# Optimization experiments

Hardware: AMD Instinct MI355X
Metric: run time of the kernel (lower is better)

Reference implementation:

```python
import jax, jax.numpy as jnp
import numpy as np

D_MODEL, N_HEADS, D_LLM = 1024, 16, 4096
D_KEYS = D_MODEL // N_HEADS  # 64


def setup_inputs() -> dict:
    key = jax.random.key(0)
    ks = jax.random.split(key, 11)
    s = lambda fan_in: 1.0 / np.sqrt(fan_in)
    inp = {
        "target_embedding": jax.random.normal(ks[0], (4, 2048, D_MODEL), jnp.float32),
        "source_embedding": jax.random.normal(ks[1], (4, 1024, D_LLM), jnp.float32),
        "value_embedding": jax.random.normal(ks[2], (4, 1024, D_LLM), jnp.float32),
        "Wq": jax.random.uniform(ks[3], (D_MODEL, D_KEYS * N_HEADS), jnp.float32, -s(D_MODEL), s(D_MODEL)),
        "bq": jax.random.uniform(ks[4], (D_KEYS * N_HEADS,), jnp.float32, -s(D_MODEL), s(D_MODEL)),
        "Wk": jax.random.uniform(ks[5], (D_LLM, D_KEYS * N_HEADS), jnp.float32, -s(D_LLM), s(D_LLM)),
        "bk": jax.random.uniform(ks[6], (D_KEYS * N_HEADS,), jnp.float32, -s(D_LLM), s(D_LLM)),
        "Wv": jax.random.uniform(ks[7], (D_LLM, D_KEYS * N_HEADS), jnp.float32, -s(D_LLM), s(D_LLM)),
        "bv": jax.random.uniform(ks[8], (D_KEYS * N_HEADS,), jnp.float32, -s(D_LLM), s(D_LLM)),
        "Wo": jax.random.uniform(ks[9], (D_KEYS * N_HEADS, D_MODEL), jnp.float32, -s(D_KEYS * N_HEADS), s(D_KEYS * N_HEADS)),
        "bo": jax.random.uniform(ks[10], (D_MODEL,), jnp.float32, -s(D_KEYS * N_HEADS), s(D_KEYS * N_HEADS)),
    }
    return inp


def reference(target_embedding, source_embedding, value_embedding,
              Wq, bq, Wk, bk, Wv, bv, Wo, bo):
    B, L, _ = target_embedding.shape
    _, S, _ = source_embedding.shape
    H, E = N_HEADS, D_KEYS
    q = (target_embedding @ Wq + bq).reshape(B, L, H, E)
    k = (source_embedding @ Wk + bk).reshape(B, S, H, E)
    v = (value_embedding @ Wv + bv).reshape(B, S, H, E)
    scale = 1.0 / np.sqrt(E)
    scores = jnp.einsum('blhe,bshe->bhls', q, k)  # [B,H,L,S]
    A = jax.nn.softmax(scale * scores, axis=-1)   # dropout = identity (eval mode)
    out = jnp.einsum('bhls,bshe->blhe', A, v).reshape(B, L, H * E)
    return out @ Wo + bo
```

## Files before the change

kernel.cpp:

```cpp
#include <hip/hip_runtime.h>
#include <hip/hip_bf16.h>

using bf16 = __hip_bfloat16;
typedef __attribute__((ext_vector_type(8))) short short8;
typedef __attribute__((ext_vector_type(4))) float f32x4;

static constexpr int Bc = 4, Lc = 2048, Sc = 1024;
static constexpr int DModel = 1024;

__device__ __forceinline__ void gload16(const void* g, void* l) {
  __builtin_amdgcn_global_load_lds((const __attribute__((address_space(1))) void*)g,
                                   (__attribute__((address_space(3))) void*)l,
                                   16, 0, 0);
}

__device__ __forceinline__ void wait_vm3()  { asm volatile("s_waitcnt vmcnt(3)" ::: "memory"); }
__device__ __forceinline__ void wait_vm0()  { asm volatile("s_waitcnt vmcnt(0)" ::: "memory"); }
__device__ __forceinline__ void barrier_raw() { asm volatile("s_barrier" ::: "memory"); }

__global__ __launch_bounds__(256) void prep(
    const float* __restrict__ Wq, bf16* __restrict__ WqT,
    const float* __restrict__ Wk, bf16* __restrict__ WkT,
    const float* __restrict__ Wv, bf16* __restrict__ WvT,
    const float* __restrict__ Wo, bf16* __restrict__ WoT,
    const float* __restrict__ a, bf16* __restrict__ ao, long na4,
    const float* __restrict__ b, bf16* __restrict__ bo, long nb4,
    const float* __restrict__ c, bf16* __restrict__ co, long nc4) {
  __shared__ bf16 tile[32][33];
  int bid = blockIdx.x;
  if (bid < 10240) {
    const float* in; bf16* out; int R, l;
    if (bid < 1024)      { in = Wq; out = WqT; R = 1024; l = bid; }
    else if (bid < 5120) { in = Wk; out = WkT; R = 4096; l = bid - 1024; }
    else if (bid < 9216) { in = Wv; out = WvT; R = 4096; l = bid - 5120; }
    else                 { in = Wo; out = WoT; R = 1024; l = bid - 9216; }
    const int C = 1024;
    int bx = l & 31, by = l >> 5;
    int tx = threadIdx.x & 31, ty = threadIdx.x >> 5;
    int r0 = by * 32, c0 = bx * 32;
#pragma unroll
    for (int i = 0; i < 32; i += 8)
      tile[ty + i][tx] = __float2bfloat16(in[(long)(r0 + ty + i) * C + c0 + tx]);
    __syncthreads();
#pragma unroll
    for (int i = 0; i < 32; i += 8)
      out[(long)(c0 + ty + i) * R + r0 + tx] = tile[tx][ty + i];
  } else {
    int cb = bid - 10240;
    long total = na4 + nb4 + nc4;
    long stride = (long)(gridDim.x - 10240) * blockDim.x;
    for (long i = (long)cb * blockDim.x + threadIdx.x; i < total; i += stride) {
      const float* src; bf16* dst; long j;
      if (i < na4)            { src = a; dst = ao; j = i; }
      else if (i < na4 + nb4) { src = b; dst = bo; j = i - na4; }
      else                    { src = c; dst = co; j = i - na4 - nb4; }
      float4 v = reinterpret_cast<const float4*>(src)[j];
      alignas(8) bf16 t[4] = {__float2bfloat16(v.x), __float2bfloat16(v.y),
                              __float2bfloat16(v.z), __float2bfloat16(v.w)};
      reinterpret_cast<ushort4*>(dst)[j] = *reinterpret_cast<const ushort4*>(t);
    }
  }
}

__device__ __forceinline__ void gemm_bal_core(const bf16* __restrict__ A, const bf16* __restrict__ Bt,
                                              const float* __restrict__ bias,
                                              bf16* __restrict__ Cb, bf16* __restrict__ Cvt,
                                              int K, int bx, int by, bf16* lds) {
  const int tid = threadIdx.x;
  const int lane = tid & 63, g = lane >> 4, lm = lane & 15;
  const int wid = tid >> 6, wr = wid >> 1, wc = wid & 1;
  const long brow = (long)by * 256, bcol = (long)bx * 128;

  char* L = (char*)lds;
  const int rowA = tid >> 2;
  const int kg = (tid & 3) ^ ((rowA >> 1) & 3);
  const bf16* aS = A + (brow + rowA) * (long)K + kg * 8;
  const bf16* bS = Bt + (bcol + rowA) * (long)K + kg * 8;
  const long aOff1 = 128l * K;
  const int dA = tid * 16;

#define STAGEB(t_) {                                                     \
    const int _b = (t_) % 3; const long _ko = (long)(t_) * 32;           \
    gload16(aS + _ko,         L + _b * 24576 + dA);                      \
    gload16(aS + aOff1 + _ko, L + _b * 24576 + 8192 + dA);               \
    gload16(bS + _ko,         L + _b * 24576 + 16384 + dA); }

  f32x4 zero = {0.f, 0.f, 0.f, 0.f};
  f32x4 acc[4][4];
#pragma unroll
  for (int i = 0; i < 4; ++i)
#pragma unroll
    for (int j = 0; j < 4; ++j) acc[i][j] = zero;

  STAGEB(0);
  STAGEB(1);

  const int nt = K >> 5;
  for (int t = 0; t < nt; ++t) {
    if (t + 1 < nt) wait_vm3();
    else            wait_vm0();
    barrier_raw();

    const char* Bf = L + (t % 3) * 24576;
    short8 aR[4], bR[4];
#pragma unroll
    for (int mi = 0; mi < 4; ++mi) {
      const int r = wr * 64 + mi * 16 + lm;
      aR[mi] = *reinterpret_cast<const short8*>(
          Bf + r * 64 + ((g ^ ((r >> 1) & 3)) << 4));
    }
#pragma unroll
    for (int ni = 0; ni < 4; ++ni) {
      const int r = wc * 64 + ni * 16 + lm;
      bR[ni] = *reinterpret_cast<const short8*>(
          Bf + 16384 + r * 64 + ((g ^ ((r >> 1) & 3)) << 4));
    }

    if (t + 2 < nt) STAGEB(t + 2);

#pragma unroll
    for (int mi = 0; mi < 4; ++mi)
#pragma unroll
      for (int ni = 0; ni < 4; ++ni)
        acc[mi][ni] = __builtin_amdgcn_mfma_f32_16x16x32_bf16(aR[mi], bR[ni], acc[mi][ni], 0, 0, 0);
  }
#undef STAGEB

#pragma unroll
  for (int ni = 0; ni < 4; ++ni) {
    long n = bcol + wc * 64 + ni * 16 + lm;
    float bv = bias ? bias[n] : 0.f;
#pragma unroll
    for (int mi = 0; mi < 4; ++mi) {
      long m0 = brow + wr * 64 + mi * 16 + g * 4;
      if (Cvt) {
        long b = m0 >> 10, s0 = m0 & 1023;
        alignas(8) bf16 t4[4];
#pragma unroll
        for (int r = 0; r < 4; ++r) t4[r] = __float2bfloat16(acc[mi][ni][r] + bv);
        *reinterpret_cast<ushort4*>(Cvt + ((b << 10) + n) * 1024 + s0) =
            *reinterpret_cast<const ushort4*>(t4);
      } else {
#pragma unroll
        for (int r = 0; r < 4; ++r)
          Cb[(m0 + r) * 1024 + n] = __float2bfloat16(acc[mi][ni][r] + bv);
      }
    }
  }
}

__global__ __launch_bounds__(512, 4) void gemm_qkv_bal(
    const bf16* __restrict__ Ak, const bf16* __restrict__ Bk, const float* __restrict__ bk_, bf16* __restrict__ Ck, int Kk, int nbk,
    const bf16* __restrict__ Av, const bf16* __restrict__ Bv_, const float* __restrict__ bv_, bf16* __restrict__ CvT, int Kv, int nbv,
    const bf16* __restrict__ Aq, const bf16* __restrict__ Bq_, const float* __restrict__ bq_, bf16* __restrict__ Cq, int Kq) {
  __shared__ bf16 lds[36864];
  int bid = blockIdx.x;
  const bf16 *A, *Bt; const float* bias; bf16 *C = nullptr, *Cvt = nullptr; int K, l, nb;
  if (bid < nbk)            { A = Ak; Bt = Bk;  bias = bk_; C = Ck;    K = Kk; l = bid;             nb = nbk; }
  else if (bid < nbk + nbv) { A = Av; Bt = Bv_; bias = bv_; Cvt = CvT; K = Kv; l = bid - nbk;       nb = nbv; }
  else                      { A = Aq; Bt = Bq_; bias = bq_; C = Cq;   K = Kq; l = bid - nbk - nbv; nb = gridDim.x - nbk - nbv; }
  int g = (l & 7) * (nb >> 3) + (l >> 3);
  gemm_bal_core(A, Bt, bias, C, Cvt, K, g & 7, g >> 3, lds);
}

__device__ __forceinline__ void gemm_core(const bf16* __restrict__ A, const bf16* __restrict__ Bt,
                                          const float* __restrict__ bias,
                                          bf16* __restrict__ Cb, float* __restrict__ Cf,
                                          int N, int K, int bx, int by,
                                          bf16* As, bf16* Bs) {
  const int tid = threadIdx.x;
  const int lane = tid & 63, g = lane >> 4, lm = lane & 15;
  const int wid = tid >> 6, wr = wid >> 1, wc = wid & 1;
  const long brow = (long)by * 128, bcol = (long)bx * 128;

  const bf16* asrc[4];
  const bf16* bsrc[4];
  int dsto[4];
#pragma unroll
  for (int t = 0; t < 4; ++t) {
    int sl = tid + t * 256;
    int row = sl >> 3;
    int kg = (sl & 7) ^ (row & 7);
    asrc[t] = A + (brow + row) * (long)K + kg * 8;
    bsrc[t] = Bt + (bcol + row) * (long)K + kg * 8;
    dsto[t] = sl * 16;
  }

  f32x4 zero = {0.f, 0.f, 0.f, 0.f};
  f32x4 acc[4][4];
#pragma unroll
  for (int i = 0; i < 4; ++i)
#pragma unroll
    for (int j = 0; j < 4; ++j) acc[i][j] = zero;

  char* Asc = (char*)As;
  char* Bsc = (char*)Bs;

#pragma unroll
  for (int t = 0; t < 4; ++t) {
    gload16(asrc[t], Asc + dsto[t]);
    gload16(bsrc[t], Bsc + dsto[t]);
    asrc[t] += 64; bsrc[t] += 64;
  }

  const int nt = K >> 6;
  for (int i = 0; i < nt; ++i) {
    wait_vm0();
    barrier_raw();

    const char* Ab = Asc + (i & 1) * 16384;
    const char* Bb = Bsc + (i & 1) * 16384;
    short8 af[2][4], bfv[2][4];
#pragma unroll
    for (int ks = 0; ks < 2; ++ks) {
#pragma unroll
      for (int mi = 0; mi < 4; ++mi) {
        int m = wr * 64 + mi * 16 + lm;
        af[ks][mi] = *reinterpret_cast<const short8*>(
            Ab + ((m * 128 + ks * 64 + g * 16) ^ ((m & 7) << 4)));
      }
#pragma unroll
      for (int ni = 0; ni < 4; ++ni) {
        int n = wc * 64 + ni * 16 + lm;
        bfv[ks][ni] = *reinterpret_cast<const short8*>(
            Bb + ((n * 128 + ks * 64 + g * 16) ^ ((n & 7) << 4)));
      }
    }

    if (i + 1 < nt) {
      const int nxt = (i + 1) & 1;
#pragma unroll
      for (int t = 0; t < 4; ++t) {
        gload16(asrc[t], Asc + nxt * 16384 + dsto[t]);
        gload16(bsrc[t], Bsc + nxt * 16384 + dsto[t]);
        asrc[t] += 64; bsrc[t] += 64;
      }
    }

#pragma unroll
    for (int ks = 0; ks < 2; ++ks)
#pragma unroll
      for (int mi = 0; mi < 4; ++mi)
#pragma unroll
        for (int ni = 0; ni < 4; ++ni)
          acc[mi][ni] = __builtin_amdgcn_mfma_f32_16x16x32_bf16(af[ks][mi], bfv[ks][ni], acc[mi][ni], 0, 0, 0);
  }

#pragma unroll
  for (int ni = 0; ni < 4; ++ni) {
    long n = bcol + wc * 64 + ni * 16 + lm;
    float bv = bias ? bias[n] : 0.f;
#pragma unroll
    for (int mi = 0; mi < 4; ++mi) {
      long m0 = brow + wr * 64 + mi * 16 + g * 4;
#pragma unroll
      for (int r = 0; r < 4; ++r) {
        float o = acc[mi][ni][r] + bv;
        if (Cb) Cb[(m0 + r) * N + n] = __float2bfloat16(o);
        else    Cf[(m0 + r) * N + n] = o;
      }
    }
  }
}

__global__ __launch_bounds__(256) void gemm_bt(const bf16* __restrict__ A,
                                               const bf16* __restrict__ Bt,
                                               const float* __restrict__ bias,
                                               bf16* __restrict__ Cb,
                                               float* __restrict__ Cf,
                                               int N, int K) {
  __shared__ bf16 As[2 * 128 * 64];
  __shared__ bf16 Bs[2 * 128 * 64];
  int bid = blockIdx.x;
  int g = (bid & 7) * (gridDim.x >> 3) + (bid >> 3);
  gemm_core(A, Bt, bias, Cb, Cf, N, K, g & 7, g >> 3, As, Bs);
}

__global__ __launch_bounds__(512) void attn_fused(const bf16* __restrict__ q,
                                                  const bf16* __restrict__ k,
                                                  const bf16* __restrict__ vT,
                                                  bf16* __restrict__ o) {
  constexpr float C2 = 0.18033688011112042f;
  constexpr float THR = 6.0f;
  __shared__ bf16 Kl[2][64 * 64];
  __shared__ bf16 Vl[2][64 * 64];
  __shared__ bf16 Pl[8][16 * 64];
  const int tid = threadIdx.x;
  const int lane = tid & 63, g = lane >> 4, lm = lane & 15;
  const int wid = tid >> 6;
  int bid = blockIdx.x;
  int gl = (bid & 7) * 128 + (bid >> 3);
  const int qt = gl & 15, bh = gl >> 4;
  const int b = bh >> 4, h = bh & 15;
  const int qbase = qt * 128 + wid * 16;

  const bf16* qrow = q + (long)(b * Lc + qbase + lm) * DModel + h * 64;
  short8 qa0 = *reinterpret_cast<const short8*>(qrow + g * 8);
  short8 qa1 = *reinterpret_cast<const short8*>(qrow + 32 + g * 8);
#pragma unroll
  for (int j = 0; j < 8; ++j) {
    union { ushort u; bf16 h; } cv;
    cv.u = (ushort)qa0[j];
    bf16 s0 = __float2bfloat16(__bfloat162float(cv.h) * C2);
    qa0[j] = (short)*reinterpret_cast<ushort*>(&s0);
    cv.u = (ushort)qa1[j];
    bf16 s1 = __float2bfloat16(__bfloat162float(cv.h) * C2);
    qa1[j] = (short)*reinterpret_cast<ushort*>(&s1);
  }

  const bf16* kbase = k + (long)b * Sc * DModel + h * 64;
  const bf16* vbase = vT + ((long)b * DModel + h * 64) * Sc;

  const int srow = tid >> 3;
  const int scg = (tid & 7) ^ (srow & 7);
  const bf16* ksrc = kbase + (long)srow * DModel + scg * 8;
  const bf16* vsrc = vbase + (long)srow * Sc + scg * 8;
  const int dsto = tid * 16;

  f32x4 zero = {0.f, 0.f, 0.f, 0.f};
  f32x4 accO[4];
#pragma unroll
  for (int i = 0; i < 4; ++i) accO[i] = zero;
  f32x4 accL = zero;
  float mst[4] = {-1e30f, -1e30f, -1e30f, -1e30f};

  short8 vones;
#pragma unroll
  for (int j = 0; j < 8; ++j) vones[j] = (short)0x3F80;

  char* Klc = (char*)Kl;
  char* Vlc = (char*)Vl;
  char* Plc = (char*)Pl + wid * (16 * 64 * 2);

  gload16(ksrc, Klc + dsto);
  gload16(vsrc, Vlc + dsto);
  ksrc += 64 * DModel; vsrc += 64;

  for (int j = 0; j < Sc / 64; ++j) {
    const int cur = j & 1;
    wait_vm0();
    barrier_raw();
    if (j + 1 < Sc / 64) {
      const int nxt = cur ^ 1;
      gload16(ksrc, Klc + nxt * 8192 + dsto);
      gload16(vsrc, Vlc + nxt * 8192 + dsto);
      ksrc += 64 * DModel; vsrc += 64;
    }

    const char* Kb = Klc + cur * 8192;
    const char* Vb = Vlc + cur * 8192;

    f32x4 scv[4];
    __builtin_amdgcn_s_setprio(1);
#pragma unroll
    for (int st = 0; st < 4; ++st) {
      int s = st * 16 + lm;
      int sw = (s & 7) << 4;
      short8 kb0 = *reinterpret_cast<const short8*>(Kb + ((s * 128 + g * 16) ^ sw));
      short8 kb1 = *reinterpret_cast<const short8*>(Kb + ((s * 128 + 64 + g * 16) ^ sw));
      f32x4 z = zero;
      z = __builtin_amdgcn_mfma_f32_16x16x32_bf16(qa0, kb0, z, 0, 0, 0);
      z = __builtin_amdgcn_mfma_f32_16x16x32_bf16(qa1, kb1, z, 0, 0, 0);
      scv[st] = z;
    }
    __builtin_amdgcn_s_setprio(0);

    float pmax[4];
#pragma unroll
    for (int r = 0; r < 4; ++r)
      pmax[r] = fmaxf(fmaxf(scv[0][r], scv[1][r]), fmaxf(scv[2][r], scv[3][r]));
    int need = 0;
#pragma unroll
    for (int r = 0; r < 4; ++r) need |= (pmax[r] > mst[r] + THR) ? 1 : 0;
    if (__any(need)) {
#pragma unroll
      for (int r = 0; r < 4; ++r) {
        float mx = pmax[r];
        mx = fmaxf(mx, __shfl_xor(mx, 1));
        mx = fmaxf(mx, __shfl_xor(mx, 2));
        mx = fmaxf(mx, __shfl_xor(mx, 4));
        mx = fmaxf(mx, __shfl_xor(mx, 8));
        float mnew = fmaxf(mst[r], mx);
        float corr = __builtin_amdgcn_exp2f(mst[r] - mnew);
        mst[r] = mnew;
        accL[r] *= corr;
#pragma unroll
        for (int et = 0; et < 4; ++et) accO[et][r] *= corr;
      }
    }
#pragma unroll
    for (int r = 0; r < 4; ++r) {
      int qq = g * 4 + r;
      int swp = (qq & 7) << 4;
#pragma unroll
      for (int st = 0; st < 4; ++st) {
        float p = __builtin_amdgcn_exp2f(scv[st][r] - mst[r]);
        *reinterpret_cast<bf16*>(Plc + ((qq * 128 + (st * 16 + lm) * 2) ^ swp)) =
            __float2bfloat16(p);
      }
    }

    __builtin_amdgcn_s_setprio(1);
#pragma unroll
    for (int sk = 0; sk < 2; ++sk) {
      short8 pa = *reinterpret_cast<const short8*>(
          Plc + ((lm * 128 + sk * 64 + g * 16) ^ ((lm & 7) << 4)));
      accL = __builtin_amdgcn_mfma_f32_16x16x32_bf16(pa, vones, accL, 0, 0, 0);
#pragma unroll
      for (int et = 0; et < 4; ++et) {
        int e = et * 16 + lm;
        short8 vb = *reinterpret_cast<const short8*>(
            Vb + ((e * 128 + sk * 64 + g * 16) ^ ((e & 7) << 4)));
        accO[et] = __builtin_amdgcn_mfma_f32_16x16x32_bf16(pa, vb, accO[et], 0, 0, 0);
      }
    }
    __builtin_amdgcn_s_setprio(0);
  }

#pragma unroll
  for (int r = 0; r < 4; ++r) {
    float inv = 1.0f / accL[r];
    long row = (long)(b * Lc + qbase + g * 4 + r);
#pragma unroll
    for (int et = 0; et < 4; ++et)
      o[row * DModel + h * 64 + et * 16 + lm] = __float2bfloat16(accO[et][r] * inv);
  }
}

extern "C" void kernel_launch(void* const* d_in, const int* in_sizes, int n_in,
                              void* d_out, int out_size, void* d_ws, size_t ws_size,
                              hipStream_t stream) {
  const float* tgt = (const float*)d_in[0];
  const float* src = (const float*)d_in[1];
  const float* val = (const float*)d_in[2];
  const float* Wq  = (const float*)d_in[3];
  const float* bq  = (const float*)d_in[4];
  const float* Wk  = (const float*)d_in[5];
  const float* bk  = (const float*)d_in[6];
  const float* Wv  = (const float*)d_in[7];
  const float* bv  = (const float*)d_in[8];
  const float* Wo  = (const float*)d_in[9];
  const float* bo  = (const float*)d_in[10];
  float* out = (float*)d_out;
  char* ws = (char*)d_ws;

  const long n4_tgt = (long)8192 * 1024 / 4;
  const long n4_sv  = (long)4096 * 4096 / 4;

  if (ws_size < (132ul << 20)) return;

  bf16* WqT  = (bf16*)(ws + (0l   << 20));
  bf16* WkT  = (bf16*)(ws + (2l   << 20));
  bf16* WvT  = (bf16*)(ws + (10l  << 20));
  bf16* WoT  = (bf16*)(ws + (18l  << 20));
  bf16* tgtb = (bf16*)(ws + (20l  << 20));
  bf16* srcb = (bf16*)(ws + (36l  << 20));
  bf16* valb = (bf16*)(ws + (68l  << 20));
  bf16* qb   = (bf16*)(ws + (100l << 20));
  bf16* kb   = (bf16*)(ws + (116l << 20));
  bf16* vTb  = (bf16*)(ws + (124l << 20));
  bf16* attnb = tgtb;

  prep<<<10240 + 4096, 256, 0, stream>>>(Wq, WqT, Wk, WkT, Wv, WvT, Wo, WoT,
                                         tgt, tgtb, n4_tgt, src, srcb, n4_sv,
                                         val, valb, n4_sv);
  gemm_qkv_bal<<<512, 512, 0, stream>>>(srcb, WkT, bk, kb, 4096, 128,
                                        valb, WvT, bv, vTb, 4096, 128,
                                        tgtb, WqT, bq, qb, 1024);
  attn_fused<<<1024, 512, 0, stream>>>(qb, kb, vTb, attnb);
  gemm_bt<<<512, 256, 0, stream>>>(attnb, WoT, bo, (bf16*)nullptr, out, 1024, 1024);
}
```

Measured before the change: 220.0 us.

## Retile QKV GEMM to 256x64 blocks with 256 threads and double buffering

Replaces the 256x128 tile, 512-thread, triple-buffered QKV projection GEMM with a 256x64 tile, 256-thread kernel that double-buffers LDS and waits for all loads each iteration. Each wave now covers 64 rows against the full 64-column B tile, and the grid doubles to 1024 blocks. The goal is better occupancy and load balance across CUs from smaller LDS use and more blocks. In exchange, each block reuses less data (more global traffic for A per output) and the prefetch depth drops from two stages to one, which exposes more memory latency.

```diff
diff --git a/kernel.cpp b/kernel.cpp
--- a/kernel.cpp
+++ b/kernel.cpp
@@ -14,7 +14,6 @@
                                    16, 0, 0);
 }
 
-__device__ __forceinline__ void wait_vm3()  { asm volatile("s_waitcnt vmcnt(3)" ::: "memory"); }
 __device__ __forceinline__ void wait_vm0()  { asm volatile("s_waitcnt vmcnt(0)" ::: "memory"); }
 __device__ __forceinline__ void barrier_raw() { asm volatile("s_barrier" ::: "memory"); }
 
@@ -62,28 +61,37 @@
   }
 }
 
-__device__ __forceinline__ void gemm_bal_core(const bf16* __restrict__ A, const bf16* __restrict__ Bt,
-                                              const float* __restrict__ bias,
-                                              bf16* __restrict__ Cb, bf16* __restrict__ Cvt,
-                                              int K, int bx, int by, bf16* lds) {
+__device__ __forceinline__ void gemm64_core(const bf16* __restrict__ A, const bf16* __restrict__ Bt,
+                                            const float* __restrict__ bias,
+                                            bf16* __restrict__ Cb, bf16* __restrict__ Cvt,
+                                            int K, int bx, int by, bf16* lds) {
   const int tid = threadIdx.x;
   const int lane = tid & 63, g = lane >> 4, lm = lane & 15;
-  const int wid = tid >> 6, wr = wid >> 1, wc = wid & 1;
-  const long brow = (long)by * 256, bcol = (long)bx * 128;
+  const int wid = tid >> 6;
+  const long brow = (long)by * 256, bcol = (long)bx * 64;
 
   char* L = (char*)lds;
-  const int rowA = tid >> 2;
-  const int kg = (tid & 3) ^ ((rowA >> 1) & 3);
-  const bf16* aS = A + (brow + rowA) * (long)K + kg * 8;
-  const bf16* bS = Bt + (bcol + rowA) * (long)K + kg * 8;
-  const long aOff1 = 128l * K;
-  const int dA = tid * 16;
-
-#define STAGEB(t_) {                                                     \
-    const int _b = (t_) % 3; const long _ko = (long)(t_) * 32;           \
-    gload16(aS + _ko,         L + _b * 24576 + dA);                      \
-    gload16(aS + aOff1 + _ko, L + _b * 24576 + 8192 + dA);               \
-    gload16(bS + _ko,         L + _b * 24576 + 16384 + dA); }
+  const bf16* aS[4]; int dA[4];
+#pragma unroll
+  for (int j = 0; j < 4; ++j) {
+    int sl = tid + j * 256;
+    int row = sl >> 2;
+    int kg = (sl & 3) ^ ((row >> 1) & 3);
+    aS[j] = A + (brow + row) * (long)K + kg * 8;
+    dA[j] = sl * 16;
+  }
+  const int rowB = tid >> 2;
+  const int kgB = (tid & 3) ^ ((rowB >> 1) & 3);
+  const bf16* bS = Bt + (bcol + rowB) * (long)K + kgB * 8;
+  const int dB = 16384 + tid * 16;
+
+#define STAGE64(t_) {                                                     \
+    const int _b = ((t_) & 1) * 20480; const long _ko = (long)(t_) * 32;  \
+    gload16(aS[0] + _ko, L + _b + dA[0]);                                 \
+    gload16(aS[1] + _ko, L + _b + dA[1]);                                 \
+    gload16(aS[2] + _ko, L + _b + dA[2]);                                 \
+    gload16(aS[3] + _ko, L + _b + dA[3]);                                 \
+    gload16(bS + _ko,    L + _b + dB); }
 
   f32x4 zero = {0.f, 0.f, 0.f, 0.f};
   f32x4 acc[4][4];
@@ -92,31 +100,29 @@
 #pragma unroll
     for (int j = 0; j < 4; ++j) acc[i][j] = zero;
 
-  STAGEB(0);
-  STAGEB(1);
+  STAGE64(0);
 
   const int nt = K >> 5;
   for (int t = 0; t < nt; ++t) {
-    if (t + 1 < nt) wait_vm3();
-    else            wait_vm0();
+    wait_vm0();
     barrier_raw();
 
-    const char* Bf = L + (t % 3) * 24576;
+    const char* Bf = L + (t & 1) * 20480;
     short8 aR[4], bR[4];
 #pragma unroll
     for (int mi = 0; mi < 4; ++mi) {
-      const int r = wr * 64 + mi * 16 + lm;
+      const int r = wid * 64 + mi * 16 + lm;
       aR[mi] = *reinterpret_cast<const short8*>(
           Bf + r * 64 + ((g ^ ((r >> 1) & 3)) << 4));
     }
 #pragma unroll
     for (int ni = 0; ni < 4; ++ni) {
-      const int r = wc * 64 + ni * 16 + lm;
+      const int r = ni * 16 + lm;
       bR[ni] = *reinterpret_cast<const short8*>(
           Bf + 16384 + r * 64 + ((g ^ ((r >> 1) & 3)) << 4));
     }
 
-    if (t + 2 < nt) STAGEB(t + 2);
+    if (t + 1 < nt) STAGE64(t + 1);
 
 #pragma unroll
     for (int mi = 0; mi < 4; ++mi)
@@ -124,15 +130,15 @@
       for (int ni = 0; ni < 4; ++ni)
         acc[mi][ni] = __builtin_amdgcn_mfma_f32_16x16x32_bf16(aR[mi], bR[ni], acc[mi][ni], 0, 0, 0);
   }
-#undef STAGEB
+#undef STAGE64
 
 #pragma unroll
   for (int ni = 0; ni < 4; ++ni) {
-    long n = bcol + wc * 64 + ni * 16 + lm;
+    long n = bcol + ni * 16 + lm;
     float bv = bias ? bias[n] : 0.f;
 #pragma unroll
     for (int mi = 0; mi < 4; ++mi) {
-      long m0 = brow + wr * 64 + mi * 16 + g * 4;
+      long m0 = brow + wid * 64 + mi * 16 + g * 4;
       if (Cvt) {
         long b = m0 >> 10, s0 = m0 & 1023;
         alignas(8) bf16 t4[4];
@@ -149,18 +155,18 @@
   }
 }
 
-__global__ __launch_bounds__(512, 4) void gemm_qkv_bal(
+__global__ __launch_bounds__(256, 4) void gemm_qkv64(
     const bf16* __restrict__ Ak, const bf16* __restrict__ Bk, const float* __restrict__ bk_, bf16* __restrict__ Ck, int Kk, int nbk,
     const bf16* __restrict__ Av, const bf16* __restrict__ Bv_, const float* __restrict__ bv_, bf16* __restrict__ CvT, int Kv, int nbv,
     const bf16* __restrict__ Aq, const bf16* __restrict__ Bq_, const float* __restrict__ bq_, bf16* __restrict__ Cq, int Kq) {
-  __shared__ bf16 lds[36864];
+  __shared__ bf16 lds[20480];
   int bid = blockIdx.x;
   const bf16 *A, *Bt; const float* bias; bf16 *C = nullptr, *Cvt = nullptr; int K, l, nb;
   if (bid < nbk)            { A = Ak; Bt = Bk;  bias = bk_; C = Ck;    K = Kk; l = bid;             nb = nbk; }
   else if (bid < nbk + nbv) { A = Av; Bt = Bv_; bias = bv_; Cvt = CvT; K = Kv; l = bid - nbk;       nb = nbv; }
   else                      { A = Aq; Bt = Bq_; bias = bq_; C = Cq;   K = Kq; l = bid - nbk - nbv; nb = gridDim.x - nbk - nbv; }
   int g = (l & 7) * (nb >> 3) + (l >> 3);
-  gemm_bal_core(A, Bt, bias, C, Cvt, K, g & 7, g >> 3, lds);
+  gemm64_core(A, Bt, bias, C, Cvt, K, g & 15, g >> 4, lds);
 }
 
 __device__ __forceinline__ void gemm_core(const bf16* __restrict__ A, const bf16* __restrict__ Bt,
@@ -464,9 +470,9 @@
   prep<<<10240 + 4096, 256, 0, stream>>>(Wq, WqT, Wk, WkT, Wv, WvT, Wo, WoT,
                                          tgt, tgtb, n4_tgt, src, srcb, n4_sv,
                                          val, valb, n4_sv);
-  gemm_qkv_bal<<<512, 512, 0, stream>>>(srcb, WkT, bk, kb, 4096, 128,
-                                        valb, WvT, bv, vTb, 4096, 128,
-                                        tgtb, WqT, bq, qb, 1024);
+  gemm_qkv64<<<1024, 256, 0, stream>>>(srcb, WkT, bk, kb, 4096, 256,
+                                       valb, WvT, bv, vTb, 4096, 256,
+                                       tgtb, WqT, bq, qb, 1024);
   attn_fused<<<1024, 512, 0, stream>>>(qb, kb, vTb, attnb);
   gemm_bt<<<512, 256, 0, stream>>>(attnb, WoT, bo, (bf16*)nullptr, out, 1024, 1024);
 }
```

New measurement: 247.9 us. 1.13x slower.
